# Optimization experiments

Hardware: AMD Instinct MI355X
Metric: run time of the kernel (lower is better)

The kernel has to match this reference:

```python
import jax, jax.numpy as jnp
import numpy as np
from jax import lax

N_BANDS, TAPS, CUTOFF, BETA = 4, 62, 0.15, 9.0
B, T = 16, 262144


def make_pqmf_filters(N=N_BANDS, taps=TAPS, cutoff=CUTOFF, beta=BETA):
    # scipy.signal.firwin(taps+1, cutoff, window=('kaiser', beta)) reimplemented:
    numtaps = taps + 1
    m = np.arange(numtaps) - (numtaps - 1) / 2.0
    qmf = cutoff * np.sinc(cutoff * m) * np.kaiser(numtaps, beta)
    qmf /= qmf.sum()  # unit DC gain (firwin scale=True, lowpass)
    k = np.arange(N)[:, None]
    n = np.arange(numtaps)[None, :]
    const = (2 * k + 1) * (np.pi / (2 * N)) * (n - (taps - 1) / 2.0)
    phase = ((-1.0) ** np.arange(N))[:, None] * np.pi / 4.0
    H = 2.0 * qmf * np.cos(const + phase)
    G = 2.0 * qmf * np.cos(const - phase)
    return H.astype(np.float32), G.astype(np.float32)


def setup_inputs() -> dict:
    key = jax.random.key(0)
    x = jax.random.normal(key, (B, 1, T), dtype=jnp.float32)
    H, G = make_pqmf_filters()
    return {"x": x, "H": jnp.asarray(H), "G": jnp.asarray(G)}


def reference(x, H, G):
    # Round trip: synthesis(analysis(x)). x: (B,1,T); H,G: (N, taps+1).
    N = H.shape[0]
    pad = (H.shape[1] - 1) // 2  # taps//2 = 31
    dn = ('NCH', 'OIH', 'NCH')
    # analysis: stride-1 FIR bank then the updown_filter strided conv, which is
    # exactly take-every-Nth-sample (updown_filter[0,k,k]=1).
    sub = lax.conv_general_dilated(x, H[:, None, :], (1,), [(pad, pad)],
                                   dimension_numbers=dn)  # (B, N, T)
    sub = sub[:, :, ::N]  # (B, N, T//N)
    # synthesis: conv1d_transpose(updown_filter*N, stride N) == zero-stuff upsample
    # scaled by N; fused here via lhs_dilation. Extra N-1 right pad matches the
    # trailing zeros of the TF transpose-conv output (length T//N * N).
    recon = lax.conv_general_dilated(sub * N, G[None, :, :], (1,),
                                     [(pad, pad + N - 1)], lhs_dilation=(N,),
                                     dimension_numbers=dn)  # (B, 1, T)
    return recon
```

## Files before the change

kernel.cpp:

```cpp
#include <hip/hip_runtime.h>

#define TT 262144
#define BB 16
#define SS 65536
#define WSTRIDE 132
#define QPB 1024
#define TILEQ 1056

__global__ __launch_bounds__(256) void prep(const float* __restrict__ x,
                                            const float* __restrict__ H,
                                            const float* __restrict__ G,
                                            float* __restrict__ W,
                                            float* __restrict__ out) {
    const int blk = blockIdx.x;
    const int tid = threadIdx.x;

    if (blk >= 32) {
        int e = (blk - 32) * 256 + tid;
        if (e >= 4 * WSTRIDE) return;
        int p = e / WSTRIDE;
        int i = e % WSTRIDE;
        int dd = 126 + p - i;
        float acc = 0.f;
        if (dd >= 0 && dd <= 124) {
            int j0 = (3 - p) & 3;
            for (int k = 0; k < 4; ++k) {
                for (int j = j0; j <= 62; j += 4) {
                    int a = 124 - j - dd;
                    if (a >= 0 && a <= 62) acc += H[k * 63 + a] * G[k * 63 + j];
                }
            }
        }
        W[e] = 4.0f * acc;
        return;
    }

    const int q_local = tid >> 4;
    const int s_idx = tid & 15;
    const int e = blk * 16 + q_local;
    const int b = e >> 5;
    const int idx = e & 31;
    const int u = (idx < 16) ? idx : (SS - 32 + idx);
    const float* xb = x + (size_t)b * TT;

    const int s = u - 7 + s_idx;
    float c0 = 0.f, c1 = 0.f, c2 = 0.f, c3 = 0.f;
    if (s >= 0 && s < SS) {
        float s0 = 0.f, s1 = 0.f, s2 = 0.f, s3 = 0.f;
        const int xbase = 4 * s - 31;
#pragma unroll
        for (int a = 0; a < 63; ++a) {
            int xi = xbase + a;
            float xv = (xi >= 0 && xi < TT) ? xb[xi] : 0.f;
            s0 += xv * H[a];
            s1 += xv * H[63 + a];
            s2 += xv * H[126 + a];
            s3 += xv * H[189 + a];
        }
        const int d4 = 4 * (s - u);
        {
            int j = d4 + 31;
            if (j <= 62) c0 = s0 * G[j] + s1 * G[63 + j] + s2 * G[126 + j] + s3 * G[189 + j];
        }
        {
            int j = d4 + 30;
            c1 = s0 * G[j] + s1 * G[63 + j] + s2 * G[126 + j] + s3 * G[189 + j];
        }
        {
            int j = d4 + 29;
            c2 = s0 * G[j] + s1 * G[63 + j] + s2 * G[126 + j] + s3 * G[189 + j];
        }
        {
            int j = d4 + 28;
            c3 = s0 * G[j] + s1 * G[63 + j] + s2 * G[126 + j] + s3 * G[189 + j];
        }
    }
#pragma unroll
    for (int m = 8; m >= 1; m >>= 1) {
        c0 += __shfl_xor(c0, m);
        c1 += __shfl_xor(c1, m);
        c2 += __shfl_xor(c2, m);
        c3 += __shfl_xor(c3, m);
    }
    if (s_idx == 0) {
        float4 v = make_float4(4.f * c0, 4.f * c1, 4.f * c2, 4.f * c3);
        reinterpret_cast<float4*>(out + (size_t)b * TT)[u] = v;
    }
}

__global__ __launch_bounds__(256) void pqmf_fused(const float* __restrict__ x,
                                                  const float* __restrict__ W,
                                                  float* __restrict__ out) {
    __shared__ float4 xs4[TILEQ];
    __shared__ float4 ws4[132];

    const int tid = threadIdx.x;
    const int b = blockIdx.y;
    const int Q0 = blockIdx.x * QPB;
    const float4* X4 = reinterpret_cast<const float4*>(x + (size_t)b * TT);

    const int gq0 = Q0 - 16;
    for (int j = tid; j < TILEQ; j += 256) {
        int gq = gq0 + j;
        xs4[j] = (gq >= 0 && gq < SS) ? X4[gq] : make_float4(0.f, 0.f, 0.f, 0.f);
    }
    if (tid < 132) ws4[tid] = reinterpret_cast<const float4*>(W)[tid];
    __syncthreads();

    const int w = tid >> 6, l = tid & 63;
    const int base = w * 256 + l;

    float4 a0 = make_float4(0.f, 0.f, 0.f, 0.f);
    float4 a1 = a0, a2 = a0, a3 = a0;

#define ACCUM(ar, xv)                                                          \
    ar.x = fmaf(W0.w, xv.w, fmaf(W0.z, xv.z, fmaf(W0.y, xv.y, fmaf(W0.x, xv.x, ar.x)))); \
    ar.y = fmaf(W1.w, xv.w, fmaf(W1.z, xv.z, fmaf(W1.y, xv.y, fmaf(W1.x, xv.x, ar.y)))); \
    ar.z = fmaf(W2.w, xv.w, fmaf(W2.z, xv.z, fmaf(W2.y, xv.y, fmaf(W2.x, xv.x, ar.z)))); \
    ar.w = fmaf(W3.w, xv.w, fmaf(W3.z, xv.z, fmaf(W3.y, xv.y, fmaf(W3.x, xv.x, ar.w))));

#pragma unroll 2
    for (int c = 0; c < 33; ++c) {
        float4 W0 = ws4[c];
        float4 W1 = ws4[33 + c];
        float4 W2 = ws4[66 + c];
        float4 W3 = ws4[99 + c];
        float4 xv0 = xs4[base + c];
        float4 xv1 = xs4[base + 64 + c];
        float4 xv2 = xs4[base + 128 + c];
        float4 xv3 = xs4[base + 192 + c];
        ACCUM(a0, xv0)
        ACCUM(a1, xv1)
        ACCUM(a2, xv2)
        ACCUM(a3, xv3)
    }
#undef ACCUM

    float4* ob4 = reinterpret_cast<float4*>(out + (size_t)b * TT);
    const int u0 = Q0 + base;
    if ((unsigned)(u0 - 16) < (unsigned)(SS - 32)) ob4[u0] = a0;
    if ((unsigned)(u0 + 64 - 16) < (unsigned)(SS - 32)) ob4[u0 + 64] = a1;
    if ((unsigned)(u0 + 128 - 16) < (unsigned)(SS - 32)) ob4[u0 + 128] = a2;
    if ((unsigned)(u0 + 192 - 16) < (unsigned)(SS - 32)) ob4[u0 + 192] = a3;
}

extern "C" void kernel_launch(void* const* d_in, const int* in_sizes, int n_in,
                              void* d_out, int out_size, void* d_ws, size_t ws_size,
                              hipStream_t stream) {
    const float* x = (const float*)d_in[0];
    const float* H = (const float*)d_in[1];
    const float* G = (const float*)d_in[2];
    float* outp = (float*)d_out;
    float* W = (float*)d_ws;

    hipLaunchKernelGGL(prep, dim3(35), dim3(256), 0, stream, x, H, G, W, outp);
    hipLaunchKernelGGL(pqmf_fused, dim3(SS / QPB, BB), dim3(256), 0, stream,
                       x, W, outp);
}
```

Before: 32.96 us.

## Move edge handling into main kernel and parallelize weight prep across four lanes

The boundary-sample computation moves out of the prep kernel and into the first and last blocks of the main kernel, where it reads x from the already-loaded shared tile instead of global memory. The prep kernel now only builds the combined polyphase weights, splitting the sum over the band index across four lanes and reducing with shuffles, so it is shorter on the critical path. The main kernel reads weights straight from global (cached, uniform) memory instead of staging them in LDS, and the unroll factor goes from 2 to 3. The risk is extra work and register pressure in the edge blocks, which could make them a tail.

```diff
diff --git a/kernel.cpp b/kernel.cpp
--- a/kernel.cpp
+++ b/kernel.cpp
@@ -3,96 +3,44 @@
 #define TT 262144
 #define BB 16
 #define SS 65536
-#define WSTRIDE 132
 #define QPB 1024
 #define TILEQ 1056
 
-__global__ __launch_bounds__(256) void prep(const float* __restrict__ x,
-                                            const float* __restrict__ H,
-                                            const float* __restrict__ G,
-                                            float* __restrict__ W,
-                                            float* __restrict__ out) {
-    const int blk = blockIdx.x;
-    const int tid = threadIdx.x;
-
-    if (blk >= 32) {
-        int e = (blk - 32) * 256 + tid;
-        if (e >= 4 * WSTRIDE) return;
-        int p = e / WSTRIDE;
-        int i = e % WSTRIDE;
+__global__ __launch_bounds__(256) void prep_w(const float* __restrict__ H,
+                                              const float* __restrict__ G,
+                                              float* __restrict__ W) {
+    int t = blockIdx.x * 256 + threadIdx.x;
+    int e = t >> 2;
+    int k = t & 3;
+    bool valid = (e < 4 * 132);
+    float acc = 0.f;
+    if (valid) {
+        int p = e / 132;
+        int i = e % 132;
         int dd = 126 + p - i;
-        float acc = 0.f;
         if (dd >= 0 && dd <= 124) {
             int j0 = (3 - p) & 3;
-            for (int k = 0; k < 4; ++k) {
-                for (int j = j0; j <= 62; j += 4) {
+#pragma unroll
+            for (int jj = 0; jj < 16; ++jj) {
+                int j = j0 + 4 * jj;
+                if (j <= 62) {
                     int a = 124 - j - dd;
                     if (a >= 0 && a <= 62) acc += H[k * 63 + a] * G[k * 63 + j];
                 }
             }
         }
-        W[e] = 4.0f * acc;
-        return;
     }
-
-    const int q_local = tid >> 4;
-    const int s_idx = tid & 15;
-    const int e = blk * 16 + q_local;
-    const int b = e >> 5;
-    const int idx = e & 31;
-    const int u = (idx < 16) ? idx : (SS - 32 + idx);
-    const float* xb = x + (size_t)b * TT;
-
-    const int s = u - 7 + s_idx;
-    float c0 = 0.f, c1 = 0.f, c2 = 0.f, c3 = 0.f;
-    if (s >= 0 && s < SS) {
-        float s0 = 0.f, s1 = 0.f, s2 = 0.f, s3 = 0.f;
-        const int xbase = 4 * s - 31;
-#pragma unroll
-        for (int a = 0; a < 63; ++a) {
-            int xi = xbase + a;
-            float xv = (xi >= 0 && xi < TT) ? xb[xi] : 0.f;
-            s0 += xv * H[a];
-            s1 += xv * H[63 + a];
-            s2 += xv * H[126 + a];
-            s3 += xv * H[189 + a];
-        }
-        const int d4 = 4 * (s - u);
-        {
-            int j = d4 + 31;
-            if (j <= 62) c0 = s0 * G[j] + s1 * G[63 + j] + s2 * G[126 + j] + s3 * G[189 + j];
-        }
-        {
-            int j = d4 + 30;
-            c1 = s0 * G[j] + s1 * G[63 + j] + s2 * G[126 + j] + s3 * G[189 + j];
-        }
-        {
-            int j = d4 + 29;
-            c2 = s0 * G[j] + s1 * G[63 + j] + s2 * G[126 + j] + s3 * G[189 + j];
-        }
-        {
-            int j = d4 + 28;
-            c3 = s0 * G[j] + s1 * G[63 + j] + s2 * G[126 + j] + s3 * G[189 + j];
-        }
-    }
-#pragma unroll
-    for (int m = 8; m >= 1; m >>= 1) {
-        c0 += __shfl_xor(c0, m);
-        c1 += __shfl_xor(c1, m);
-        c2 += __shfl_xor(c2, m);
-        c3 += __shfl_xor(c3, m);
-    }
-    if (s_idx == 0) {
-        float4 v = make_float4(4.f * c0, 4.f * c1, 4.f * c2, 4.f * c3);
-        reinterpret_cast<float4*>(out + (size_t)b * TT)[u] = v;
-    }
+    acc += __shfl_xor(acc, 1);
+    acc += __shfl_xor(acc, 2);
+    if (valid && k == 0) W[e] = 4.0f * acc;
 }
 
 __global__ __launch_bounds__(256) void pqmf_fused(const float* __restrict__ x,
-                                                  const float* __restrict__ W,
+                                                  const float* __restrict__ Wg,
+                                                  const float* __restrict__ H,
+                                                  const float* __restrict__ G,
                                                   float* __restrict__ out) {
     __shared__ float4 xs4[TILEQ];
-    __shared__ float4 ws4[132];
 
     const int tid = threadIdx.x;
     const int b = blockIdx.y;
@@ -104,7 +52,6 @@
         int gq = gq0 + j;
         xs4[j] = (gq >= 0 && gq < SS) ? X4[gq] : make_float4(0.f, 0.f, 0.f, 0.f);
     }
-    if (tid < 132) ws4[tid] = reinterpret_cast<const float4*>(W)[tid];
     __syncthreads();
 
     const int w = tid >> 6, l = tid & 63;
@@ -113,18 +60,20 @@
     float4 a0 = make_float4(0.f, 0.f, 0.f, 0.f);
     float4 a1 = a0, a2 = a0, a3 = a0;
 
+    const float4* W4 = reinterpret_cast<const float4*>(Wg);
+
 #define ACCUM(ar, xv)                                                          \
     ar.x = fmaf(W0.w, xv.w, fmaf(W0.z, xv.z, fmaf(W0.y, xv.y, fmaf(W0.x, xv.x, ar.x)))); \
     ar.y = fmaf(W1.w, xv.w, fmaf(W1.z, xv.z, fmaf(W1.y, xv.y, fmaf(W1.x, xv.x, ar.y)))); \
     ar.z = fmaf(W2.w, xv.w, fmaf(W2.z, xv.z, fmaf(W2.y, xv.y, fmaf(W2.x, xv.x, ar.z)))); \
     ar.w = fmaf(W3.w, xv.w, fmaf(W3.z, xv.z, fmaf(W3.y, xv.y, fmaf(W3.x, xv.x, ar.w))));
 
-#pragma unroll 2
+#pragma unroll 3
     for (int c = 0; c < 33; ++c) {
-        float4 W0 = ws4[c];
-        float4 W1 = ws4[33 + c];
-        float4 W2 = ws4[66 + c];
-        float4 W3 = ws4[99 + c];
+        float4 W0 = W4[c];
+        float4 W1 = W4[33 + c];
+        float4 W2 = W4[66 + c];
+        float4 W3 = W4[99 + c];
         float4 xv0 = xs4[base + c];
         float4 xv1 = xs4[base + 64 + c];
         float4 xv2 = xs4[base + 128 + c];
@@ -142,6 +91,57 @@
     if ((unsigned)(u0 + 64 - 16) < (unsigned)(SS - 32)) ob4[u0 + 64] = a1;
     if ((unsigned)(u0 + 128 - 16) < (unsigned)(SS - 32)) ob4[u0 + 128] = a2;
     if ((unsigned)(u0 + 192 - 16) < (unsigned)(SS - 32)) ob4[u0 + 192] = a3;
+
+    const bool edgeLo = (blockIdx.x == 0);
+    const bool edgeHi = (blockIdx.x == gridDim.x - 1);
+    if (edgeLo || edgeHi) {
+        const int q_local = tid >> 4;
+        const int s_idx = tid & 15;
+        const int u = edgeLo ? q_local : (SS - 16 + q_local);
+        const int s = u - 7 + s_idx;
+        float c0 = 0.f, c1 = 0.f, c2 = 0.f, c3 = 0.f;
+        if (s >= 0 && s < SS) {
+            const float* xsf = reinterpret_cast<const float*>(xs4);
+            const int lbase = 4 * s - 31 - 4 * Q0 + 64;
+            float s0 = 0.f, s1 = 0.f, s2 = 0.f, s3 = 0.f;
+#pragma unroll
+            for (int a = 0; a < 63; ++a) {
+                float xv = xsf[lbase + a];
+                s0 += xv * H[a];
+                s1 += xv * H[63 + a];
+                s2 += xv * H[126 + a];
+                s3 += xv * H[189 + a];
+            }
+            const int d4 = 4 * (s - u);
+            {
+                int j = d4 + 31;
+                if (j <= 62) c0 = s0 * G[j] + s1 * G[63 + j] + s2 * G[126 + j] + s3 * G[189 + j];
+            }
+            {
+                int j = d4 + 30;
+                c1 = s0 * G[j] + s1 * G[63 + j] + s2 * G[126 + j] + s3 * G[189 + j];
+            }
+            {
+                int j = d4 + 29;
+                c2 = s0 * G[j] + s1 * G[63 + j] + s2 * G[126 + j] + s3 * G[189 + j];
+            }
+            {
+                int j = d4 + 28;
+                c3 = s0 * G[j] + s1 * G[63 + j] + s2 * G[126 + j] + s3 * G[189 + j];
+            }
+        }
+#pragma unroll
+        for (int m = 8; m >= 1; m >>= 1) {
+            c0 += __shfl_xor(c0, m);
+            c1 += __shfl_xor(c1, m);
+            c2 += __shfl_xor(c2, m);
+            c3 += __shfl_xor(c3, m);
+        }
+        if (s_idx == 0) {
+            float4 v = make_float4(4.f * c0, 4.f * c1, 4.f * c2, 4.f * c3);
+            ob4[u] = v;
+        }
+    }
 }
 
 extern "C" void kernel_launch(void* const* d_in, const int* in_sizes, int n_in,
@@ -153,7 +153,7 @@
     float* outp = (float*)d_out;
     float* W = (float*)d_ws;
 
-    hipLaunchKernelGGL(prep, dim3(35), dim3(256), 0, stream, x, H, G, W, outp);
+    hipLaunchKernelGGL(prep_w, dim3(9), dim3(256), 0, stream, H, G, W);
     hipLaunchKernelGGL(pqmf_fused, dim3(SS / QPB, BB), dim3(256), 0, stream,
-                       x, W, outp);
+                       x, W, H, G, outp);
 }
```

Result: faster. 27.28 us (-17.2%).
